# Performance work log

Hardware: AMD Instinct MI355X
Metric: run time of the kernel (lower is better)

Reference implementation:

```python
import jax, jax.numpy as jnp
import numpy as np

B, L, H, Q = 64, 512, 1024, 64
VA_H = 256


def setup_inputs() -> dict:
    key = jax.random.key(0)
    ks = jax.random.split(key, 10)
    hidden_states = jax.random.normal(ks[0], (B, L, H), dtype=jnp.float32)
    quad_spans = jax.random.randint(ks[1], (B, Q, 4), 0, L, dtype=jnp.int64)
    quad_mask = jnp.ones((B, Q), dtype=jnp.int32)
    s = 0.02
    W1 = jax.random.normal(ks[2], (3 * H, VA_H), dtype=jnp.float32) * s
    b1 = jnp.zeros((VA_H,), dtype=jnp.float32)
    W2 = jax.random.normal(ks[3], (VA_H, VA_H // 2), dtype=jnp.float32) * s
    b2 = jnp.zeros((VA_H // 2,), dtype=jnp.float32)
    W3 = jax.random.normal(ks[4], (VA_H // 2, 2), dtype=jnp.float32) * s
    b3 = jnp.zeros((2,), dtype=jnp.float32)
    return {"hidden_states": hidden_states, "quad_spans": quad_spans,
            "quad_mask": quad_mask, "W1": W1, "b1": b1, "W2": W2, "b2": b2,
            "W3": W3, "b3": b3}


def _pool_spans(hidden_states, quad_spans, quad_mask):
    # hidden_states [B,L,H]; quad_spans [B,Q,4]; quad_mask [B,Q]
    Bn, Ln, Hn = hidden_states.shape
    pos = jnp.arange(Ln)[None, None, :]                      # [1,1,L]
    asp_s = quad_spans[:, :, 0:1]
    asp_e = quad_spans[:, :, 1:2]
    opi_s = quad_spans[:, :, 2:3]
    opi_e = quad_spans[:, :, 3:4]
    asp_valid = asp_s >= 2
    opi_valid = opi_s >= 2
    sep = pos == 1                                           # [SEP] fallback
    asp_m = ((pos >= asp_s) & (pos <= asp_e) & asp_valid) | (~asp_valid & sep)
    opi_m = ((pos >= opi_s) & (pos <= opi_e) & opi_valid) | (~opi_valid & sep)
    qm = (quad_mask != 0)[:, :, None]
    asp_f = (asp_m & qm).astype(hidden_states.dtype)         # [B,Q,L]
    opi_f = (opi_m & qm).astype(hidden_states.dtype)
    h_asp = jnp.einsum('bql,blh->bqh', asp_f, hidden_states) / jnp.clip(
        asp_f.sum(-1, keepdims=True), 1.0, None)
    h_opi = jnp.einsum('bql,blh->bqh', opi_f, hidden_states) / jnp.clip(
        opi_f.sum(-1, keepdims=True), 1.0, None)
    return h_asp, h_opi


def reference(hidden_states, quad_spans, quad_mask, W1, b1, W2, b2, W3, b3):
    h_asp, h_opi = _pool_spans(hidden_states, quad_spans, quad_mask)
    h_pair = jnp.concatenate([h_asp, h_opi, h_asp * h_opi], axis=-1)  # [B,Q,3H]
    x = jax.nn.gelu(h_pair @ W1 + b1, approximate=False)   # torch GELU = exact
    x = jax.nn.gelu(x @ W2 + b2, approximate=False)        # dropout: eval mode
    x = x @ W3 + b3                                        # [B,Q,2]
    va = jax.nn.sigmoid(x) * 8.0 + 1.0
    return va * quad_mask[:, :, None].astype(va.dtype)
```

## Files before the change

### kernel.cpp

```cpp
#include <hip/hip_runtime.h>
#include <math.h>


typedef __attribute__((ext_vector_type(4))) float f32x4;
typedef __attribute__((ext_vector_type(8))) short bf16x8;

#define NPAIR 4096
#define LSEQ 512
#define HDIM 1024

#if defined(__has_builtin)
#if __has_builtin(__builtin_amdgcn_global_load_lds)
#define HAVE_GLDS 1
#endif
#endif
#ifndef HAVE_GLDS
#define HAVE_GLDS 0
#endif

__device__ __forceinline__ unsigned int pack2(float lo, float hi) {
  const unsigned int a = __float_as_uint(lo) + 0x8000u;
  const unsigned int b = __float_as_uint(hi) + 0x8000u;
  return __builtin_amdgcn_perm(b, a, 0x07060302u);
}
__device__ __forceinline__ unsigned short f2bf(float f) {
  return (unsigned short)((__float_as_uint(f) + 0x8000u) >> 16);
}
__device__ __forceinline__ float gelu(float x) {
  return 0.5f * x * (1.f + erff(x * 0.70710678118654752f));
}

__global__ __launch_bounds__(256, 4) void pool_mfma_kernel(
    const float* __restrict__ hs, const int* __restrict__ spans,
    const int* __restrict__ qmask, unsigned short* __restrict__ hpair) {
  __shared__ __align__(16) unsigned char smem[34816];
  __shared__ float scl[128];
  typedef unsigned short BlT[64][40];
  BlT* Bl = (BlT*)smem;
  float(*S)[68] = (float(*)[68])smem;

  const int b = blockIdx.x >> 4;
  const int n0 = (blockIdx.x & 15) * 64;
  const int tid = threadIdx.x;
  const int lane = tid & 63;
  const int lm = lane & 15, quad = lane >> 4;
  const int wm = (tid >> 6) * 32;

  const bool is64 =
      (spans[1] == 0) && (spans[3] == 0) && (spans[5] == 0) && (spans[7] == 0);

  auto span_of = [&](int r, int& s, int& e) {
    const int q = r & 63, t = r >> 6;
    const int idx = (b * 64 + q) * 4 + t * 2;
    s = is64 ? spans[idx * 2] : spans[idx];
    e = is64 ? spans[idx * 2 + 2] : spans[idx + 1];
    if (s < 2) { s = 1; e = 1; }
  };
  int s0, e0, s1, e1;
  span_of(wm + lm, s0, e0);
  span_of(wm + 16 + lm, s1, e1);

  if (tid < 128) {
    int s, e;
    span_of(tid, s, e);
    const int c = (e >= s) ? (e - s + 1) : 0;
    const float sc = 1.f / (float)(c < 1 ? 1 : c);
    scl[tid] = (qmask[b * 64 + (tid & 63)] != 0) ? sc : 0.f;
  }

  f32x4 acc[2][4];
#pragma unroll
  for (int f = 0; f < 2; ++f)
#pragma unroll
    for (int g = 0; g < 4; ++g) acc[f][g] = f32x4{0.f, 0.f, 0.f, 0.f};

  const float* hsb = hs + (size_t)b * (LSEQ * HDIM);
  const int nl = tid & 63;
  const int kw = (tid >> 6) * 8;

  auto load8 = [&](int kbase, unsigned int (&tmp)[4]) {
    const float* src = hsb + (size_t)(kbase + kw) * HDIM + n0 + nl;
#pragma unroll
    for (int i = 0; i < 4; ++i) {
      const float f0 = src[(size_t)(2 * i) * HDIM];
      const float f1 = src[(size_t)(2 * i + 1) * HDIM];
      tmp[i] = pack2(f0, f1);
    }
  };

  unsigned int tmp[4];
  load8(0, tmp);
  *(uint4*)&Bl[0][nl][kw] = make_uint4(tmp[0], tmp[1], tmp[2], tmp[3]);

  for (int it = 0; it < 16; ++it) {
    const int k0 = it * 32;
    __syncthreads();
    if (it < 15) load8(k0 + 32, tmp);

    bf16x8 a0, a1;
#pragma unroll
    for (int j = 0; j < 8; ++j) {
      const int k = k0 + quad * 8 + j;
      a0[j] = (short)((k >= s0 && k <= e0) ? 0x3F80 : 0);
      a1[j] = (short)((k >= s1 && k <= e1) ? 0x3F80 : 0);
    }
    const BlT& Bc = Bl[it & 1];
#pragma unroll
    for (int g = 0; g < 4; ++g) {
      bf16x8 bg = *(const bf16x8*)&Bc[g * 16 + lm][quad * 8];
      acc[0][g] = __builtin_amdgcn_mfma_f32_16x16x32_bf16(a0, bg, acc[0][g], 0, 0, 0);
      acc[1][g] = __builtin_amdgcn_mfma_f32_16x16x32_bf16(a1, bg, acc[1][g], 0, 0, 0);
    }
    if (it < 15) {
      *(uint4*)&Bl[(it + 1) & 1][nl][kw] = make_uint4(tmp[0], tmp[1], tmp[2], tmp[3]);
    }
  }

  __syncthreads();
#pragma unroll
  for (int f = 0; f < 2; ++f)
#pragma unroll
    for (int g = 0; g < 4; ++g)
#pragma unroll
      for (int r = 0; r < 4; ++r)
        S[wm + f * 16 + quad * 4 + r][g * 16 + lm] = acc[f][g][r];
  __syncthreads();

  const int q = tid >> 2;
  const int cg = (tid & 3) * 16;
  const float sA = scl[q], sO = scl[64 + q];
  unsigned short* dst = hpair + (size_t)(b * 64 + q) * 3072 + n0 + cg;
#pragma unroll
  for (int h = 0; h < 2; ++h) {
    float a[8], o[8];
#pragma unroll
    for (int i = 0; i < 8; ++i) {
      a[i] = S[q][cg + h * 8 + i] * sA;
      o[i] = S[64 + q][cg + h * 8 + i] * sO;
    }
    uint4 wa, wo, wp;
    wa.x = pack2(a[0], a[1]); wa.y = pack2(a[2], a[3]);
    wa.z = pack2(a[4], a[5]); wa.w = pack2(a[6], a[7]);
    wo.x = pack2(o[0], o[1]); wo.y = pack2(o[2], o[3]);
    wo.z = pack2(o[4], o[5]); wo.w = pack2(o[6], o[7]);
    wp.x = pack2(a[0] * o[0], a[1] * o[1]); wp.y = pack2(a[2] * o[2], a[3] * o[3]);
    wp.z = pack2(a[4] * o[4], a[5] * o[5]); wp.w = pack2(a[6] * o[6], a[7] * o[7]);
    *(uint4*)(dst + h * 8) = wa;
    *(uint4*)(dst + 1024 + h * 8) = wo;
    *(uint4*)(dst + 2048 + h * 8) = wp;
  }
}

__global__ void transpose_two(const float* __restrict__ W1,
                              unsigned short* __restrict__ W1T,
                              const float* __restrict__ W2,
                              unsigned short* __restrict__ W2T) {
  __shared__ float t[32][33];
  const float* in;
  unsigned short* out;
  int R, C, c0, r0;
  int blk = blockIdx.x;
  if (blk < 768) {
    in = W1; out = W1T; R = 3072; C = 256;
    c0 = (blk & 7) * 32; r0 = (blk >> 3) * 32;
  } else {
    blk -= 768;
    in = W2; out = W2T; R = 256; C = 128;
    c0 = (blk & 3) * 32; r0 = (blk >> 2) * 32;
  }
  const int x = threadIdx.x, y = threadIdx.y;
#pragma unroll
  for (int i = 0; i < 32; i += 8)
    t[y + i][x] = in[(size_t)(r0 + y + i) * C + c0 + x];
  __syncthreads();
#pragma unroll
  for (int i = 0; i < 32; i += 8)
    out[(size_t)(c0 + y + i) * R + r0 + x] = f2bf(t[x][y + i]);
}

__global__ __launch_bounds__(256) void gemm_bt_partial(
    const unsigned short* __restrict__ A, const unsigned short* __restrict__ Bt,
    float* __restrict__ P, int M, int N, int K, int KH) {
  __shared__ __align__(16) unsigned short Al[64][32];
  __shared__ __align__(16) unsigned short Bl[64][32];
  const int bm = blockIdx.x * 64, bn = blockIdx.y * 64;
  const int kz = blockIdx.z * KH;
  const int tid = threadIdx.x;
  const int wave = tid >> 6, lane = tid & 63;
  const int wm = (wave & 1) * 32, wn = (wave >> 1) * 32;
  const int lm = lane & 15, lk = (lane >> 4) * 8;

  const int srow = wave * 16 + (lane >> 2);
  const int scol = (lane & 3) * 8;
  const unsigned short* ga = A + (size_t)(bm + srow) * K + kz + scol;
  const unsigned short* gb = Bt + (size_t)(bn + srow) * K + kz + scol;
  unsigned short* la = &Al[0][0] + wave * 512;
  unsigned short* lb = &Bl[0][0] + wave * 512;

  f32x4 acc00 = {0.f, 0.f, 0.f, 0.f}, acc01 = {0.f, 0.f, 0.f, 0.f};
  f32x4 acc10 = {0.f, 0.f, 0.f, 0.f}, acc11 = {0.f, 0.f, 0.f, 0.f};

  for (int k0 = 0; k0 < KH; k0 += 32) {
#if HAVE_GLDS
    __builtin_amdgcn_global_load_lds(ga + k0, la, 16, 0, 0);
    __builtin_amdgcn_global_load_lds(gb + k0, lb, 16, 0, 0);
#else
    *(uint4*)(la + lane * 8) = *(const uint4*)(ga + k0);
    *(uint4*)(lb + lane * 8) = *(const uint4*)(gb + k0);
#endif
    __syncthreads();
    bf16x8 a0 = *(const bf16x8*)&Al[wm + lm][lk];
    bf16x8 a1 = *(const bf16x8*)&Al[wm + 16 + lm][lk];
    bf16x8 b0 = *(const bf16x8*)&Bl[wn + lm][lk];
    bf16x8 b1 = *(const bf16x8*)&Bl[wn + 16 + lm][lk];
    acc00 = __builtin_amdgcn_mfma_f32_16x16x32_bf16(a0, b0, acc00, 0, 0, 0);
    acc01 = __builtin_amdgcn_mfma_f32_16x16x32_bf16(a0, b1, acc01, 0, 0, 0);
    acc10 = __builtin_amdgcn_mfma_f32_16x16x32_bf16(a1, b0, acc10, 0, 0, 0);
    acc11 = __builtin_amdgcn_mfma_f32_16x16x32_bf16(a1, b1, acc11, 0, 0, 0);
    __syncthreads();
  }

  float* Pz = P + (size_t)blockIdx.z * M * N;
  const int r0 = bm + wm + ((lane >> 4) << 2);
  const int c0 = bn + wn + lm;
  auto emit = [&](f32x4 v, int row0, int col) {
#pragma unroll
    for (int r = 0; r < 4; ++r) Pz[(size_t)(row0 + r) * N + col] = v[r];
  };
  emit(acc00, r0, c0);
  emit(acc10, r0 + 16, c0);
  emit(acc01, r0, c0 + 16);
  emit(acc11, r0 + 16, c0 + 16);
}

__global__ __launch_bounds__(256) void reduce_bias_gelu(
    const float* __restrict__ P, const float* __restrict__ bias,
    unsigned short* __restrict__ X) {
  const int t = blockIdx.x * 256 + threadIdx.x;
  const int e = t * 4;
  float4 p0 = *(const float4*)(P + e);
  float4 p1 = *(const float4*)(P + (size_t)NPAIR * 256 + e);
  float4 bs = *(const float4*)(bias + (e & 255));
  const float v0 = gelu(p0.x + p1.x + bs.x);
  const float v1 = gelu(p0.y + p1.y + bs.y);
  const float v2 = gelu(p0.z + p1.z + bs.z);
  const float v3 = gelu(p0.w + p1.w + bs.w);
  uint2 w;
  w.x = pack2(v0, v1);
  w.y = pack2(v2, v3);
  *(uint2*)(X + e) = w;
}

__global__ __launch_bounds__(256) void gemm2_head_kernel(
    const unsigned short* __restrict__ A, const unsigned short* __restrict__ Bt,
    const float* __restrict__ b2, const float* __restrict__ W3,
    const float* __restrict__ b3, const int* __restrict__ qmask,
    float* __restrict__ out) {
  __shared__ __align__(16) unsigned short Al[64][40];
  __shared__ __align__(16) unsigned short Bl[128][40];
  __shared__ float S2[64][129];
  __shared__ float w3[256];

  const int bm = blockIdx.x * 64;
  const int tid = threadIdx.x;
  const int wave = tid >> 6, lane = tid & 63;
  const int wm = (wave & 1) * 32, wn = (wave >> 1) * 64;
  const int ar = tid >> 2, ac = (tid & 3) * 8;
  const int br = tid >> 1, bc = (tid & 1) * 16;
  const int lm = lane & 15, quad = lane >> 4;

  w3[tid] = W3[tid];

  f32x4 acc[2][4];
#pragma unroll
  for (int f = 0; f < 2; ++f)
#pragma unroll
    for (int g = 0; g < 4; ++g) acc[f][g] = f32x4{0.f, 0.f, 0.f, 0.f};

  const unsigned short* pa = A + (size_t)(bm + ar) * 256 + ac;
  const unsigned short* pb = Bt + (size_t)br * 256 + bc;

  for (int k0 = 0; k0 < 256; k0 += 32) {
    uint4 va = *(const uint4*)(pa + k0);
    uint4 vb0 = *(const uint4*)(pb + k0);
    uint4 vb1 = *(const uint4*)(pb + k0 + 8);
    *(uint4*)&Al[ar][ac] = va;
    *(uint4*)&Bl[br][bc] = vb0;
    *(uint4*)&Bl[br][bc + 8] = vb1;
    __syncthreads();
    bf16x8 a0 = *(const bf16x8*)&Al[wm + lm][quad * 8];
    bf16x8 a1 = *(const bf16x8*)&Al[wm + 16 + lm][quad * 8];
#pragma unroll
    for (int g = 0; g < 4; ++g) {
      bf16x8 bg = *(const bf16x8*)&Bl[wn + g * 16 + lm][quad * 8];
      acc[0][g] = __builtin_amdgcn_mfma_f32_16x16x32_bf16(a0, bg, acc[0][g], 0, 0, 0);
      acc[1][g] = __builtin_amdgcn_mfma_f32_16x16x32_bf16(a1, bg, acc[1][g], 0, 0, 0);
    }
    __syncthreads();
  }

#pragma unroll
  for (int f = 0; f < 2; ++f)
#pragma unroll
    for (int g = 0; g < 4; ++g) {
      const int col = wn + g * 16 + lm;
#pragma unroll
      for (int r = 0; r < 4; ++r) {
        const int row = wm + f * 16 + quad * 4 + r;
        S2[row][col] = gelu(acc[f][g][r] + b2[col]);
      }
    }
  __syncthreads();

  if (tid < 128) {
    const int row = tid >> 1, o = tid & 1;
    float a = b3[o];
#pragma unroll 8
    for (int c = 0; c < 128; ++c) a += S2[row][c] * w3[c * 2 + o];
    const int pair = bm + row;
    const float qmf = (float)qmask[pair];
    out[pair * 2 + o] = ((1.f / (1.f + expf(-a))) * 8.f + 1.f) * qmf;
  }
}

extern "C" void kernel_launch(void* const* d_in, const int* in_sizes, int n_in,
                              void* d_out, int out_size, void* d_ws,
                              size_t ws_size, hipStream_t stream) {
  const float* hs = (const float*)d_in[0];
  const int* spans = (const int*)d_in[1];
  const int* qmask = (const int*)d_in[2];
  const float* W1 = (const float*)d_in[3];
  const float* b1 = (const float*)d_in[4];
  const float* W2 = (const float*)d_in[5];
  const float* b2 = (const float*)d_in[6];
  const float* W3 = (const float*)d_in[7];
  const float* b3 = (const float*)d_in[8];
  float* out = (float*)d_out;

  const size_t HPAIR_B = 25165824;
  const size_t X1_B = 2097152;
  const size_t P_B = 8388608;
  const size_t W1T_B = 1572864;

  char* ws = (char*)d_ws;
  size_t off = 0;
  unsigned short* hpair = (unsigned short*)(ws + off); off += HPAIR_B;
  unsigned short* x1 = (unsigned short*)(ws + off);    off += X1_B;
  float* P = (float*)(ws + off);                       off += P_B;
  unsigned short* W1T = (unsigned short*)(ws + off);   off += W1T_B;
  unsigned short* W2T = (unsigned short*)(ws + off);

  transpose_two<<<800, dim3(32, 8), 0, stream>>>(W1, W1T, W2, W2T);
  pool_mfma_kernel<<<1024, 256, 0, stream>>>(hs, spans, qmask, hpair);
  gemm_bt_partial<<<dim3(64, 4, 2), 256, 0, stream>>>(hpair, W1T, P, NPAIR,
                                                      256, 3072, 1536);
  reduce_bias_gelu<<<1024, 256, 0, stream>>>(P, b1, x1);
  gemm2_head_kernel<<<64, 256, 0, stream>>>(x1, W2T, b2, W3, b3, qmask, out);
}
```

Measured before the change: 250.4 us.

## Fuse split-K reduce, GELU, and layer-2/3 head into one tail kernel

Merges the split-K partial-sum reduction with bias and GELU, the second GEMM, and the output head into a single kernel with 16-row tiles across 256 blocks. Each block converts and transposes W2 into LDS itself, so the separate W2 transpose and the bf16 intermediate x1 buffer go away. This removes a launch and a global round trip of the layer-1 activations, and raises block count from 64 to 256. In exchange, every block redundantly reads all of W2 (64 KB fp32) with strided loads, and LDS use per block goes up.

```diff
diff --git a/kernel.cpp b/kernel.cpp
--- a/kernel.cpp
+++ b/kernel.cpp
@@ -151,31 +151,19 @@
   }
 }
 
-__global__ void transpose_two(const float* __restrict__ W1,
-                              unsigned short* __restrict__ W1T,
-                              const float* __restrict__ W2,
-                              unsigned short* __restrict__ W2T) {
+__global__ void transpose_w1(const float* __restrict__ W1,
+                             unsigned short* __restrict__ W1T) {
   __shared__ float t[32][33];
-  const float* in;
-  unsigned short* out;
-  int R, C, c0, r0;
-  int blk = blockIdx.x;
-  if (blk < 768) {
-    in = W1; out = W1T; R = 3072; C = 256;
-    c0 = (blk & 7) * 32; r0 = (blk >> 3) * 32;
-  } else {
-    blk -= 768;
-    in = W2; out = W2T; R = 256; C = 128;
-    c0 = (blk & 3) * 32; r0 = (blk >> 2) * 32;
-  }
+  const int R = 3072, C = 256;
+  const int c0 = (blockIdx.x & 7) * 32, r0 = (blockIdx.x >> 3) * 32;
   const int x = threadIdx.x, y = threadIdx.y;
 #pragma unroll
   for (int i = 0; i < 32; i += 8)
-    t[y + i][x] = in[(size_t)(r0 + y + i) * C + c0 + x];
+    t[y + i][x] = W1[(size_t)(r0 + y + i) * C + c0 + x];
   __syncthreads();
 #pragma unroll
   for (int i = 0; i < 32; i += 8)
-    out[(size_t)(c0 + y + i) * R + r0 + x] = f2bf(t[x][y + i]);
+    W1T[(size_t)(c0 + y + i) * R + r0 + x] = f2bf(t[x][y + i]);
 }
 
 __global__ __launch_bounds__(256) void gemm_bt_partial(
@@ -233,93 +221,96 @@
   emit(acc11, r0 + 16, c0 + 16);
 }
 
-__global__ __launch_bounds__(256) void reduce_bias_gelu(
-    const float* __restrict__ P, const float* __restrict__ bias,
-    unsigned short* __restrict__ X) {
-  const int t = blockIdx.x * 256 + threadIdx.x;
-  const int e = t * 4;
-  float4 p0 = *(const float4*)(P + e);
-  float4 p1 = *(const float4*)(P + (size_t)NPAIR * 256 + e);
-  float4 bs = *(const float4*)(bias + (e & 255));
-  const float v0 = gelu(p0.x + p1.x + bs.x);
-  const float v1 = gelu(p0.y + p1.y + bs.y);
-  const float v2 = gelu(p0.z + p1.z + bs.z);
-  const float v3 = gelu(p0.w + p1.w + bs.w);
-  uint2 w;
-  w.x = pack2(v0, v1);
-  w.y = pack2(v2, v3);
-  *(uint2*)(X + e) = w;
-}
-
-__global__ __launch_bounds__(256) void gemm2_head_kernel(
-    const unsigned short* __restrict__ A, const unsigned short* __restrict__ Bt,
-    const float* __restrict__ b2, const float* __restrict__ W3,
-    const float* __restrict__ b3, const int* __restrict__ qmask,
-    float* __restrict__ out) {
-  __shared__ __align__(16) unsigned short Al[64][40];
-  __shared__ __align__(16) unsigned short Bl[128][40];
-  __shared__ float S2[64][129];
+__global__ __launch_bounds__(256) void tail_kernel(
+    const float* __restrict__ P, const float* __restrict__ b1,
+    const float* __restrict__ W2, const float* __restrict__ b2,
+    const float* __restrict__ W3, const float* __restrict__ b3,
+    const int* __restrict__ qmask, float* __restrict__ out) {
+  __shared__ __align__(16) unsigned short Bl[128 * 264];
+  __shared__ __align__(16) unsigned short Al[16 * 264];
+  __shared__ float S2[16][132];
   __shared__ float w3[256];
 
-  const int bm = blockIdx.x * 64;
+  const int m0 = blockIdx.x * 16;
   const int tid = threadIdx.x;
   const int wave = tid >> 6, lane = tid & 63;
-  const int wm = (wave & 1) * 32, wn = (wave >> 1) * 64;
-  const int ar = tid >> 2, ac = (tid & 3) * 8;
-  const int br = tid >> 1, bc = (tid & 1) * 16;
   const int lm = lane & 15, quad = lane >> 4;
+  const int wn = wave * 32;
 
   w3[tid] = W3[tid];
 
-  f32x4 acc[2][4];
-#pragma unroll
-  for (int f = 0; f < 2; ++f)
-#pragma unroll
-    for (int g = 0; g < 4; ++g) acc[f][g] = f32x4{0.f, 0.f, 0.f, 0.f};
-
-  const unsigned short* pa = A + (size_t)(bm + ar) * 256 + ac;
-  const unsigned short* pb = Bt + (size_t)br * 256 + bc;
-
-  for (int k0 = 0; k0 < 256; k0 += 32) {
-    uint4 va = *(const uint4*)(pa + k0);
-    uint4 vb0 = *(const uint4*)(pb + k0);
-    uint4 vb1 = *(const uint4*)(pb + k0 + 8);
-    *(uint4*)&Al[ar][ac] = va;
-    *(uint4*)&Bl[br][bc] = vb0;
-    *(uint4*)&Bl[br][bc + 8] = vb1;
-    __syncthreads();
-    bf16x8 a0 = *(const bf16x8*)&Al[wm + lm][quad * 8];
-    bf16x8 a1 = *(const bf16x8*)&Al[wm + 16 + lm][quad * 8];
-#pragma unroll
-    for (int g = 0; g < 4; ++g) {
-      bf16x8 bg = *(const bf16x8*)&Bl[wn + g * 16 + lm][quad * 8];
-      acc[0][g] = __builtin_amdgcn_mfma_f32_16x16x32_bf16(a0, bg, acc[0][g], 0, 0, 0);
-      acc[1][g] = __builtin_amdgcn_mfma_f32_16x16x32_bf16(a1, bg, acc[1][g], 0, 0, 0);
-    }
-    __syncthreads();
-  }
-
-#pragma unroll
-  for (int f = 0; f < 2; ++f)
-#pragma unroll
-    for (int g = 0; g < 4; ++g) {
-      const int col = wn + g * 16 + lm;
-#pragma unroll
-      for (int r = 0; r < 4; ++r) {
-        const int row = wm + f * 16 + quad * 4 + r;
-        S2[row][col] = gelu(acc[f][g][r] + b2[col]);
-      }
-    }
+  for (int e = tid; e < 128 * 128; e += 256) {
+    const int k2 = e >> 7;
+    const int n = e & 127;
+    const float lo = W2[(size_t)(2 * k2) * 128 + n];
+    const float hi = W2[(size_t)(2 * k2 + 1) * 128 + n];
+    *(unsigned int*)((char*)Bl + (size_t)n * 528 + k2 * 4) = pack2(lo, hi);
+  }
+
+  {
+    const int row = tid >> 4;
+    const int slot = tid & 15;
+#pragma unroll
+    for (int ss = 0; ss < 2; ++ss) {
+      const int s = slot + ss * 16;
+      const float* p0 = P + (size_t)(m0 + row) * 256 + s * 8;
+      const float* p1 = p0 + (size_t)NPAIR * 256;
+      float4 a0 = *(const float4*)p0, a1 = *(const float4*)(p0 + 4);
+      float4 c0 = *(const float4*)p1, c1 = *(const float4*)(p1 + 4);
+      float4 ba = *(const float4*)(b1 + s * 8);
+      float4 bb = *(const float4*)(b1 + s * 8 + 4);
+      const float v0 = gelu(a0.x + c0.x + ba.x);
+      const float v1 = gelu(a0.y + c0.y + ba.y);
+      const float v2 = gelu(a0.z + c0.z + ba.z);
+      const float v3 = gelu(a0.w + c0.w + ba.w);
+      const float v4 = gelu(a1.x + c1.x + bb.x);
+      const float v5 = gelu(a1.y + c1.y + bb.y);
+      const float v6 = gelu(a1.z + c1.z + bb.z);
+      const float v7 = gelu(a1.w + c1.w + bb.w);
+      uint4 w;
+      w.x = pack2(v0, v1); w.y = pack2(v2, v3);
+      w.z = pack2(v4, v5); w.w = pack2(v6, v7);
+      *(uint4*)((char*)Al + (size_t)row * 528 + s * 16) = w;
+    }
+  }
+  __syncthreads();
+
+  f32x4 acc[2];
+  acc[0] = f32x4{0.f, 0.f, 0.f, 0.f};
+  acc[1] = f32x4{0.f, 0.f, 0.f, 0.f};
+#pragma unroll
+  for (int ks = 0; ks < 8; ++ks) {
+    bf16x8 a = *(const bf16x8*)((char*)Al + (size_t)lm * 528 + ks * 64 + quad * 16);
+#pragma unroll
+    for (int g = 0; g < 2; ++g) {
+      const int n = wn + g * 16 + lm;
+      bf16x8 b = *(const bf16x8*)((char*)Bl + (size_t)n * 528 + ks * 64 + quad * 16);
+      acc[g] = __builtin_amdgcn_mfma_f32_16x16x32_bf16(a, b, acc[g], 0, 0, 0);
+    }
+  }
+
+#pragma unroll
+  for (int g = 0; g < 2; ++g) {
+    const int col = wn + g * 16 + lm;
+    const float bc = b2[col];
+#pragma unroll
+    for (int r = 0; r < 4; ++r) S2[quad * 4 + r][col] = gelu(acc[g][r] + bc);
+  }
   __syncthreads();
 
   if (tid < 128) {
-    const int row = tid >> 1, o = tid & 1;
-    float a = b3[o];
+    const int row = tid >> 3, o = (tid >> 2) & 1, q4 = tid & 3;
+    float part = 0.f;
 #pragma unroll 8
-    for (int c = 0; c < 128; ++c) a += S2[row][c] * w3[c * 2 + o];
-    const int pair = bm + row;
-    const float qmf = (float)qmask[pair];
-    out[pair * 2 + o] = ((1.f / (1.f + expf(-a))) * 8.f + 1.f) * qmf;
+    for (int c = q4; c < 128; c += 4) part += S2[row][c] * w3[c * 2 + o];
+    part += __shfl_xor(part, 1);
+    part += __shfl_xor(part, 2);
+    if (q4 == 0) {
+      const int pair = m0 + row;
+      const float a = part + b3[o];
+      const float qmf = (float)qmask[pair];
+      out[pair * 2 + o] = ((1.f / (1.f + expf(-a))) * 8.f + 1.f) * qmf;
+    }
   }
 }
 
@@ -338,22 +329,17 @@
   float* out = (float*)d_out;
 
   const size_t HPAIR_B = 25165824;
-  const size_t X1_B = 2097152;
   const size_t P_B = 8388608;
-  const size_t W1T_B = 1572864;
 
   char* ws = (char*)d_ws;
   size_t off = 0;
   unsigned short* hpair = (unsigned short*)(ws + off); off += HPAIR_B;
-  unsigned short* x1 = (unsigned short*)(ws + off);    off += X1_B;
   float* P = (float*)(ws + off);                       off += P_B;
-  unsigned short* W1T = (unsigned short*)(ws + off);   off += W1T_B;
-  unsigned short* W2T = (unsigned short*)(ws + off);
-
-  transpose_two<<<800, dim3(32, 8), 0, stream>>>(W1, W1T, W2, W2T);
+  unsigned short* W1T = (unsigned short*)(ws + off);
+
+  transpose_w1<<<768, dim3(32, 8), 0, stream>>>(W1, W1T);
   pool_mfma_kernel<<<1024, 256, 0, stream>>>(hs, spans, qmask, hpair);
   gemm_bt_partial<<<dim3(64, 4, 2), 256, 0, stream>>>(hpair, W1T, P, NPAIR,
                                                       256, 3072, 1536);
-  reduce_bias_gelu<<<1024, 256, 0, stream>>>(P, b1, x1);
-  gemm2_head_kernel<<<64, 256, 0, stream>>>(x1, W2T, b2, W3, b3, qmask, out);
-}
+  tail_kernel<<<256, 256, 0, stream>>>(P, b1, W2, b2, W3, b3, qmask, out);
+}
```

Result: slower. 267.6 us (+6.9%).
